# Performance work log

Measured on AMD Instinct MI355X. Metric: run time of the kernel, lower is better.

Reference implementation:

```python
import jax, jax.numpy as jnp
import numpy as np

N_ELEM = 10   # len(EnvPara.ELEMENTS)
N_ATOMS = 100000
N_DIM = 256


def setup_inputs() -> dict:
    key = jax.random.key(0)
    k = jax.random.split(key, 5)
    return {
        "input_tensor": jax.random.normal(k[0], (N_ATOMS, N_DIM), jnp.float32),
        "species": jax.random.randint(k[1], (N_ATOMS,), 0, N_ELEM, dtype=jnp.int64),
        "W1": jax.random.normal(k[2], (N_ELEM, N_DIM, N_DIM), jnp.float32) / np.sqrt(N_DIM).astype(np.float32),
        "b1": jnp.zeros((N_ELEM, N_DIM), jnp.float32),
        "W2": jax.random.normal(k[3], (N_ELEM, N_DIM, 1), jnp.float32) / np.sqrt(N_DIM).astype(np.float32),
        "b2": jnp.zeros((N_ELEM, 1), jnp.float32),
    }


def _element_linear(x, species, W, b):
    # Species-routed linear: each atom uses the weight/bias of its element.
    # Loop over the small fixed element set (N_ELEM=10) to avoid materializing
    # a [n_atoms, d_in, d_out] gathered-weight tensor.
    out = jnp.zeros((x.shape[0], W.shape[2]), dtype=x.dtype)
    for e in range(W.shape[0]):
        mask = (species == e)[:, None]                      # [n_atoms, 1]
        out = out + jnp.where(mask, x @ W[e] + b[e], jnp.zeros((), x.dtype))
    return out


def reference(input_tensor, species, W1, b1, W2, b2):
    # layer2(silu(layer1(x)))
    h = _element_linear(input_tensor, species, W1, b1)      # [n_atoms, n_dim]
    h = jax.nn.silu(h)                                      # way=0 -> plain SiLU
    return _element_linear(h, species, W2, b2)              # [n_atoms, 1]
```

## Files before the change

kernel.cpp:

```cpp
#include <hip/hip_runtime.h>
#include <hip/hip_bf16.h>
#include <stdint.h>


#define NDIM 256
#define CHUNKS 16
#define BCHUNK 16384
#define TROWS 32
#define MAXT 16
#define NB_GEMM 512

typedef __attribute__((ext_vector_type(8))) short short8;
typedef __attribute__((ext_vector_type(8))) unsigned short ushort8;
typedef __attribute__((ext_vector_type(4))) float f32x4;
typedef __attribute__((ext_vector_type(2))) unsigned u32x2;

__device__ __forceinline__ unsigned short f2bf(float f) {
  unsigned u = __float_as_uint(f);
  u = (u + 0x7FFFu + ((u >> 16) & 1u)) >> 16;
  return (unsigned short)u;
}

__device__ __forceinline__ unsigned pk2(float a, float b) {
  return (unsigned)f2bf(a) | ((unsigned)f2bf(b) << 16);
}


__global__ void convw_k(const float* __restrict__ W1, unsigned short* __restrict__ wt, int NE) {
  int t = blockIdx.x * 256 + threadIdx.x;
  if (t >= NE * 8192) return;
  int n = t & 255;
  int g = (t >> 8) & 3;
  int step = (t >> 10) & 7;
  int e = t >> 13;
  int k0 = step * 32 + g * 8;
  const float* src = W1 + ((size_t)e << 16) + (size_t)k0 * NDIM + n;
  unsigned short v[8];
  #pragma unroll
  for (int j = 0; j < 8; ++j) v[j] = f2bf(src[j * NDIM]);
  char* chunk = (char*)wt + (size_t)(e * 8 + step) * BCHUNK;
  unsigned off = ((unsigned)(n * 64 + g * 16)) ^ ((unsigned)((n & 7) << 4));
  *(ushort8*)(chunk + off) = *(ushort8*)v;
}

__global__ void bhist_k(const int* __restrict__ sp, int n, int* __restrict__ bc, int NE) {
  __shared__ int wc[4][16];
  int tid = threadIdx.x;
  int i = blockIdx.x * 256 + tid;
  int s = (i < n) ? sp[i] : -1;
  int w = tid >> 6, lane = tid & 63;
  for (int e = 0; e < NE; ++e) {
    unsigned long long m = __ballot(s == e);
    if (lane == 0) wc[w][e] = __popcll(m);
  }
  __syncthreads();
  if (tid < NE) bc[blockIdx.x * NE + tid] = wc[0][tid] + wc[1][tid] + wc[2][tid] + wc[3][tid];
}

__global__ void scan_k(const int* __restrict__ bc, int* __restrict__ bo,
                       int* __restrict__ atom_start, int* __restrict__ tile_off,
                       int* __restrict__ bstart, int nblocks, int NE) {
  __shared__ int csum[256];
  __shared__ int coff[256];
  __shared__ int stot[16];
  __shared__ int sbase[16];
  int tid = threadIdx.x;
  int per = (nblocks + CHUNKS - 1) / CHUNKS;
  int e = tid / CHUNKS, c = tid % CHUNKS;
  int b0 = c * per, b1 = b0 + per; if (b1 > nblocks) b1 = nblocks;
  if (tid < NE * CHUNKS) {
    int s = 0;
    for (int b = b0; b < b1; ++b) s += bc[b * NE + e];
    csum[tid] = s;
  }
  __syncthreads();
  if (tid < NE) {
    int r = 0;
    for (int c2 = 0; c2 < CHUNKS; ++c2) { coff[tid * CHUNKS + c2] = r; r += csum[tid * CHUNKS + c2]; }
    stot[tid] = r;
  }
  __syncthreads();
  if (tid == 0) {
    int a = 0, t = 0;
    for (int e2 = 0; e2 < NE; ++e2) {
      sbase[e2] = a;
      atom_start[e2] = a; tile_off[e2] = t;
      a += stot[e2]; t += (stot[e2] + TROWS - 1) / TROWS;
    }
    atom_start[NE] = a; tile_off[NE] = t;
    int ntl = t > 0 ? t : 1;
    int nbk[16]; int tot = 0, emax = 0;
    for (int e2 = 0; e2 < NE; ++e2) {
      int nt = tile_off[e2 + 1] - tile_off[e2];
      int v = (nt > 0) ? (int)(((long long)nt * NB_GEMM) / ntl) : 0;
      if (nt > 0 && v < 1) v = 1;
      nbk[e2] = v; tot += v;
      if (nbk[e2] > nbk[emax]) emax = e2;
    }
    nbk[emax] += NB_GEMM - tot;
    int bacc = 0;
    for (int e2 = 0; e2 < NE; ++e2) { bstart[e2] = bacc; bacc += nbk[e2]; }
    bstart[NE] = bacc;
  }
  __syncthreads();
  if (tid < NE * CHUNKS) {
    int run = sbase[e] + coff[tid];
    for (int b = b0; b < b1; ++b) { bo[b * NE + e] = run; run += bc[b * NE + e]; }
  }
}

__global__ void dscatter_k(const int* __restrict__ sp, int n, const int* __restrict__ bo,
                           int* __restrict__ sorted, int NE) {
  __shared__ int wc[4][16];
  int tid = threadIdx.x;
  int i = blockIdx.x * 256 + tid;
  int s = (i < n) ? sp[i] : -1;
  int w = tid >> 6, lane = tid & 63;
  for (int e = 0; e < NE; ++e) {
    unsigned long long m = __ballot(s == e);
    if (lane == 0) wc[w][e] = __popcll(m);
  }
  __syncthreads();
  for (int e = 0; e < NE; ++e) {
    unsigned long long m = __ballot(s == e);
    if (s == e) {
      int wpre = 0;
      for (int w2 = 0; w2 < 4; ++w2) if (w2 < w) wpre += wc[w2][e];
      int rank = __popcll(m & ((1ull << lane) - 1ull));
      sorted[bo[blockIdx.x * NE + e] + wpre + rank] = i;
    }
  }
}


__global__ __launch_bounds__(512, 1) void gemm_k(
    const float* __restrict__ x, const unsigned short* __restrict__ wt,
    const float* __restrict__ b1, const float* __restrict__ w2,
    const float* __restrict__ b2, const int* __restrict__ sorted,
    const int* __restrict__ atom_start, const int* __restrict__ tile_off,
    const int* __restrict__ bstart, float* __restrict__ out, int NE)
{
  __shared__ __align__(16) char ldsT[TROWS * 512];
  __shared__ float partLds[256];
  __shared__ int ldsAtoms[MAXT * TROWS];
  __shared__ int toffs[17], astart[17], bst[17];

  int tid = threadIdx.x, lane = tid & 63, wid = tid >> 6;
  int lr = lane & 15, lg = lane >> 4;

  if (tid <= NE) {
    toffs[tid] = tile_off[tid]; astart[tid] = atom_start[tid]; bst[tid] = bstart[tid];
  }
  __syncthreads();

  int b = blockIdx.x;
  int e = 0;
  while (b >= bst[e + 1]) ++e;
  int j = b - bst[e], nbe = bst[e + 1] - bst[e];
  int nte = toffs[e + 1] - toffs[e];
  int q = nte / nbe, r = nte % nbe;
  int cnt = q + (j < r ? 1 : 0);
  if (cnt <= 0) return;
  if (cnt > MAXT) cnt = MAXT;
  int t0 = toffs[e] + j * q + (j < r ? j : r);
  int t1 = t0 + cnt;

  {
    int rs0 = astart[e] + (t0 - toffs[e]) * TROWS;
    int rvAll = astart[e + 1] - rs0;
    for (int i = tid; i < cnt * TROWS; i += 512) {
      int rloc = (i < rvAll) ? i : (rvAll - 1);
      ldsAtoms[i] = sorted[rs0 + rloc];
    }
  }
  __syncthreads();

  short8 bf[2][8];
  float bbv[2], wvv[2];
  {
    const char* wbase = (const char*)wt + (size_t)e * 8 * BCHUNK;
    #pragma unroll
    for (int nf = 0; nf < 2; ++nf) {
      int ncol = wid * 32 + nf * 16 + lr;
      unsigned off = ((unsigned)(ncol * 64 + lg * 16)) ^ ((unsigned)((ncol & 7) << 4));
      #pragma unroll
      for (int s = 0; s < 8; ++s)
        bf[nf][s] = *(const short8*)(wbase + (size_t)s * BCHUNK + off);
      bbv[nf] = b1[(size_t)e * NDIM + ncol];
      wvv[nf] = w2[(size_t)e * NDIM + ncol];
    }
  }
  float b2v = b2[e];
  #pragma unroll
  for (int nf = 0; nf < 2; ++nf) {
    #pragma unroll
    for (int s = 0; s < 8; ++s) asm volatile("" : "+v"(bf[nf][s]));
    asm volatile("" : "+v"(bbv[nf]), "+v"(wvv[nf]));
  }

  int srow = tid >> 4;
  int skc  = tid & 15;
  unsigned swzW = (unsigned)((srow & 7) << 4);
  unsigned rbW  = (unsigned)(srow * 512 + skc * 8);
  unsigned swzA = (unsigned)((lr & 7) << 4);

  float4 xr0, xr1, xr2, xr3;
  {
    int atom = ldsAtoms[srow];
    const float* xp = x + (size_t)atom * NDIM + skc * 4;
    xr0 = *(const float4*)(xp);
    xr1 = *(const float4*)(xp + 64);
    xr2 = *(const float4*)(xp + 128);
    xr3 = *(const float4*)(xp + 192);
  }

  for (int t = t0; t < t1; ++t) {
    {
      u32x2 w;
      w[0] = pk2(xr0.x, xr0.y); w[1] = pk2(xr0.z, xr0.w);
      *(u32x2*)(ldsT + ((rbW +   0) ^ swzW)) = w;
      w[0] = pk2(xr1.x, xr1.y); w[1] = pk2(xr1.z, xr1.w);
      *(u32x2*)(ldsT + ((rbW + 128) ^ swzW)) = w;
      w[0] = pk2(xr2.x, xr2.y); w[1] = pk2(xr2.z, xr2.w);
      *(u32x2*)(ldsT + ((rbW + 256) ^ swzW)) = w;
      w[0] = pk2(xr3.x, xr3.y); w[1] = pk2(xr3.z, xr3.w);
      *(u32x2*)(ldsT + ((rbW + 384) ^ swzW)) = w;
    }
    if (t + 1 < t1) {
      int atom = ldsAtoms[(t + 1 - t0) * TROWS + srow];
      const float* xp = x + (size_t)atom * NDIM + skc * 4;
      xr0 = *(const float4*)(xp);
      xr1 = *(const float4*)(xp + 64);
      xr2 = *(const float4*)(xp + 128);
      xr3 = *(const float4*)(xp + 192);
    }

    asm volatile("s_waitcnt lgkmcnt(0)" ::: "memory");
    __builtin_amdgcn_s_barrier();
    __builtin_amdgcn_sched_barrier(0);

    f32x4 acc[2][2];
    const f32x4 zero = {0.f, 0.f, 0.f, 0.f};
    #pragma unroll
    for (int i = 0; i < 2; ++i)
      #pragma unroll
      for (int jj = 0; jj < 2; ++jj) acc[i][jj] = zero;

    #pragma unroll
    for (int step = 0; step < 8; ++step) {
      short8 af[2];
      #pragma unroll
      for (int mf = 0; mf < 2; ++mf) {
        unsigned off = ((unsigned)((mf * 16 + lr) * 512 + step * 64 + lg * 16)) ^ swzA;
        af[mf] = *(const short8*)(ldsT + off);
      }
      #pragma unroll
      for (int mf = 0; mf < 2; ++mf)
        #pragma unroll
        for (int nf = 0; nf < 2; ++nf)
          acc[mf][nf] = __builtin_amdgcn_mfma_f32_16x16x32_bf16(af[mf], bf[nf][step], acc[mf][nf], 0, 0, 0);
    }

    float psum[2][4];
    #pragma unroll
    for (int mf = 0; mf < 2; ++mf)
      #pragma unroll
      for (int rg = 0; rg < 4; ++rg) psum[mf][rg] = 0.f;

    #pragma unroll
    for (int nf = 0; nf < 2; ++nf) {
      #pragma unroll
      for (int mf = 0; mf < 2; ++mf)
        #pragma unroll
        for (int rg = 0; rg < 4; ++rg) {
          float h = acc[mf][nf][rg] + bbv[nf];
          float sv = h * __builtin_amdgcn_rcpf(1.f + __expf(-h));
          psum[mf][rg] += sv * wvv[nf];
        }
    }
    #pragma unroll
    for (int mf = 0; mf < 2; ++mf)
      #pragma unroll
      for (int rg = 0; rg < 4; ++rg) {
        float v = psum[mf][rg];
        v += __shfl_xor(v, 1, 64);
        v += __shfl_xor(v, 2, 64);
        v += __shfl_xor(v, 4, 64);
        v += __shfl_xor(v, 8, 64);
        psum[mf][rg] = v;
      }
    if (lr == 0) {
      #pragma unroll
      for (int mf = 0; mf < 2; ++mf)
        #pragma unroll
        for (int rg = 0; rg < 4; ++rg)
          partLds[wid * TROWS + mf * 16 + lg * 4 + rg] = psum[mf][rg];
    }

    asm volatile("s_waitcnt lgkmcnt(0)" ::: "memory");
    __builtin_amdgcn_s_barrier();
    __builtin_amdgcn_sched_barrier(0);

    if (lane < 4) {
      int rloc = wid * 4 + lane;
      float s = b2v;
      #pragma unroll
      for (int w = 0; w < 8; ++w) s += partLds[w * TROWS + rloc];
      out[ldsAtoms[(t - t0) * TROWS + rloc]] = s;
    }
  }
}


extern "C" void kernel_launch(void* const* d_in, const int* in_sizes, int n_in,
                              void* d_out, int out_size, void* d_ws, size_t ws_size,
                              hipStream_t stream) {
  const float* x  = (const float*)d_in[0];
  const int*   sp = (const int*)d_in[1];
  const float* W1 = (const float*)d_in[2];
  const float* b1 = (const float*)d_in[3];
  const float* W2 = (const float*)d_in[4];
  const float* b2 = (const float*)d_in[5];
  float* out = (float*)d_out;

  int n_atoms = in_sizes[0] / NDIM;
  int NE = in_sizes[2] / (NDIM * NDIM);
  int nblocks = (n_atoms + 255) / 256;

  char* wsb = (char*)d_ws;
  size_t o = 0;
  int* bc = (int*)(wsb + o);         o += ((size_t)nblocks * NE * 4 + 255) & ~(size_t)255;
  int* bo = (int*)(wsb + o);         o += ((size_t)nblocks * NE * 4 + 255) & ~(size_t)255;
  int* atom_start = (int*)(wsb + o); o += 256;
  int* tile_off   = (int*)(wsb + o); o += 256;
  int* bstart     = (int*)(wsb + o); o += 256;
  int* sorted     = (int*)(wsb + o); o += ((size_t)n_atoms * 4 + 255) & ~(size_t)255;
  unsigned short* wt = (unsigned short*)(wsb + o);

  hipLaunchKernelGGL(convw_k, dim3((NE * 8192 + 255) / 256), dim3(256), 0, stream,
                     W1, wt, NE);
  hipLaunchKernelGGL(bhist_k, dim3(nblocks), dim3(256), 0, stream, sp, n_atoms, bc, NE);
  hipLaunchKernelGGL(scan_k, dim3(1), dim3(256), 0, stream, bc, bo, atom_start, tile_off,
                     bstart, nblocks, NE);
  hipLaunchKernelGGL(dscatter_k, dim3(nblocks), dim3(256), 0, stream, sp, n_atoms, bo,
                     sorted, NE);

  hipLaunchKernelGGL(gemm_k, dim3(NB_GEMM), dim3(512), 0, stream,
                     x, wt, b1, W2, b2, sorted, atom_start, tile_off, bstart, out, NE);
}
```

Measured before the change: 69.97 us.

## Double GEMM tile rows, swap MFMA operands, and stage weight conversion through LDS

The fused GEMM tile grows from 32 to 64 atom rows and the grid shrinks from 512 to 256 blocks. MFMA operands are swapped so weights form the A side and activations the B side. This lets the SiLU-dot reduction use two cross-lane shuffles instead of four, and lets b1/w2 be held per row group. The weight conversion kernel now loads W1 rows coalesced into LDS and writes transposed bf16 chunks, instead of doing strided per-thread gathers. The larger tile doubles accumulator and x-prefetch registers, and the smaller grid may leave compute units underused.

```diff
diff --git a/kernel.cpp b/kernel.cpp
--- a/kernel.cpp
+++ b/kernel.cpp
@@ -6,9 +6,9 @@
 #define NDIM 256
 #define CHUNKS 16
 #define BCHUNK 16384
-#define TROWS 32
+#define TROWS 64
 #define MAXT 16
-#define NB_GEMM 512
+#define NB_GEMM 256
 
 typedef __attribute__((ext_vector_type(8))) short short8;
 typedef __attribute__((ext_vector_type(8))) unsigned short ushort8;
@@ -27,20 +27,32 @@
 
 
 __global__ void convw_k(const float* __restrict__ W1, unsigned short* __restrict__ wt, int NE) {
-  int t = blockIdx.x * 256 + threadIdx.x;
-  if (t >= NE * 8192) return;
-  int n = t & 255;
-  int g = (t >> 8) & 3;
-  int step = (t >> 10) & 7;
-  int e = t >> 13;
-  int k0 = step * 32 + g * 8;
-  const float* src = W1 + ((size_t)e << 16) + (size_t)k0 * NDIM + n;
-  unsigned short v[8];
-  #pragma unroll
-  for (int j = 0; j < 8; ++j) v[j] = f2bf(src[j * NDIM]);
-  char* chunk = (char*)wt + (size_t)(e * 8 + step) * BCHUNK;
-  unsigned off = ((unsigned)(n * 64 + g * 16)) ^ ((unsigned)((n & 7) << 4));
-  *(ushort8*)(chunk + off) = *(ushort8*)v;
+  __shared__ float ldsW[32 * 260];
+  int blk = blockIdx.x;
+  int e = blk >> 3, step = blk & 7;
+  int tid = threadIdx.x;
+  int k0 = step * 32;
+  {
+    int kk = tid >> 3, part = tid & 7;
+    const float* src = W1 + ((size_t)e << 16) + (size_t)(k0 + kk) * NDIM + part * 32;
+    #pragma unroll
+    for (int j = 0; j < 8; ++j) {
+      float4 v = *(const float4*)(src + j * 4);
+      *(float4*)&ldsW[kk * 260 + part * 32 + j * 4] = v;
+    }
+  }
+  __syncthreads();
+  {
+    int n = tid;
+    unsigned short v[32];
+    #pragma unroll
+    for (int kk = 0; kk < 32; ++kk) v[kk] = f2bf(ldsW[kk * 260 + n]);
+    char* chunk = (char*)wt + (size_t)blk * BCHUNK;
+    unsigned swz = (unsigned)((n & 7) << 4);
+    #pragma unroll
+    for (int g = 0; g < 4; ++g)
+      *(ushort8*)(chunk + (((unsigned)(n * 64 + g * 16)) ^ swz)) = *(ushort8*)&v[g * 8];
+  }
 }
 
 __global__ void bhist_k(const int* __restrict__ sp, int n, int* __restrict__ bc, int NE) {
@@ -141,7 +153,7 @@
     const int* __restrict__ bstart, float* __restrict__ out, int NE)
 {
   __shared__ __align__(16) char ldsT[TROWS * 512];
-  __shared__ float partLds[256];
+  __shared__ float partLds[8 * TROWS];
   __shared__ int ldsAtoms[MAXT * TROWS];
   __shared__ int toffs[17], astart[17], bst[17];
 
@@ -176,137 +188,112 @@
   __syncthreads();
 
   short8 bf[2][8];
-  float bbv[2], wvv[2];
+  float bbv[2][4], wvv[2][4];
   {
     const char* wbase = (const char*)wt + (size_t)e * 8 * BCHUNK;
     #pragma unroll
-    for (int nf = 0; nf < 2; ++nf) {
-      int ncol = wid * 32 + nf * 16 + lr;
+    for (int mf = 0; mf < 2; ++mf) {
+      int ncol = wid * 32 + mf * 16 + lr;
       unsigned off = ((unsigned)(ncol * 64 + lg * 16)) ^ ((unsigned)((ncol & 7) << 4));
       #pragma unroll
       for (int s = 0; s < 8; ++s)
-        bf[nf][s] = *(const short8*)(wbase + (size_t)s * BCHUNK + off);
-      bbv[nf] = b1[(size_t)e * NDIM + ncol];
-      wvv[nf] = w2[(size_t)e * NDIM + ncol];
+        bf[mf][s] = *(const short8*)(wbase + (size_t)s * BCHUNK + off);
+      #pragma unroll
+      for (int rg = 0; rg < 4; ++rg) {
+        int n = wid * 32 + mf * 16 + lg * 4 + rg;
+        bbv[mf][rg] = b1[(size_t)e * NDIM + n];
+        wvv[mf][rg] = w2[(size_t)e * NDIM + n];
+      }
     }
   }
   float b2v = b2[e];
   #pragma unroll
-  for (int nf = 0; nf < 2; ++nf) {
-    #pragma unroll
-    for (int s = 0; s < 8; ++s) asm volatile("" : "+v"(bf[nf][s]));
-    asm volatile("" : "+v"(bbv[nf]), "+v"(wvv[nf]));
-  }
-
-  int srow = tid >> 4;
-  int skc  = tid & 15;
+  for (int mf = 0; mf < 2; ++mf)
+    #pragma unroll
+    for (int s = 0; s < 8; ++s) asm volatile("" : "+v"(bf[mf][s]));
+
+  int srow = tid >> 3;
+  int skc  = tid & 7;
   unsigned swzW = (unsigned)((srow & 7) << 4);
-  unsigned rbW  = (unsigned)(srow * 512 + skc * 8);
-  unsigned swzA = (unsigned)((lr & 7) << 4);
-
-  float4 xr0, xr1, xr2, xr3;
+  float4 xr[8];
   {
     int atom = ldsAtoms[srow];
     const float* xp = x + (size_t)atom * NDIM + skc * 4;
-    xr0 = *(const float4*)(xp);
-    xr1 = *(const float4*)(xp + 64);
-    xr2 = *(const float4*)(xp + 128);
-    xr3 = *(const float4*)(xp + 192);
+    #pragma unroll
+    for (int jj = 0; jj < 8; ++jj) xr[jj] = *(const float4*)(xp + jj * 32);
   }
 
   for (int t = t0; t < t1; ++t) {
-    {
+    #pragma unroll
+    for (int jj = 0; jj < 8; ++jj) {
       u32x2 w;
-      w[0] = pk2(xr0.x, xr0.y); w[1] = pk2(xr0.z, xr0.w);
-      *(u32x2*)(ldsT + ((rbW +   0) ^ swzW)) = w;
-      w[0] = pk2(xr1.x, xr1.y); w[1] = pk2(xr1.z, xr1.w);
-      *(u32x2*)(ldsT + ((rbW + 128) ^ swzW)) = w;
-      w[0] = pk2(xr2.x, xr2.y); w[1] = pk2(xr2.z, xr2.w);
-      *(u32x2*)(ldsT + ((rbW + 256) ^ swzW)) = w;
-      w[0] = pk2(xr3.x, xr3.y); w[1] = pk2(xr3.z, xr3.w);
-      *(u32x2*)(ldsT + ((rbW + 384) ^ swzW)) = w;
+      w[0] = pk2(xr[jj].x, xr[jj].y); w[1] = pk2(xr[jj].z, xr[jj].w);
+      *(u32x2*)(ldsT + (((unsigned)(srow * 512 + jj * 64 + skc * 8)) ^ swzW)) = w;
     }
     if (t + 1 < t1) {
       int atom = ldsAtoms[(t + 1 - t0) * TROWS + srow];
       const float* xp = x + (size_t)atom * NDIM + skc * 4;
-      xr0 = *(const float4*)(xp);
-      xr1 = *(const float4*)(xp + 64);
-      xr2 = *(const float4*)(xp + 128);
-      xr3 = *(const float4*)(xp + 192);
+      #pragma unroll
+      for (int jj = 0; jj < 8; ++jj) xr[jj] = *(const float4*)(xp + jj * 32);
     }
 
     asm volatile("s_waitcnt lgkmcnt(0)" ::: "memory");
     __builtin_amdgcn_s_barrier();
     __builtin_amdgcn_sched_barrier(0);
 
-    f32x4 acc[2][2];
+    f32x4 acc[2][4];
     const f32x4 zero = {0.f, 0.f, 0.f, 0.f};
     #pragma unroll
     for (int i = 0; i < 2; ++i)
       #pragma unroll
-      for (int jj = 0; jj < 2; ++jj) acc[i][jj] = zero;
+      for (int jj = 0; jj < 4; ++jj) acc[i][jj] = zero;
 
     #pragma unroll
     for (int step = 0; step < 8; ++step) {
-      short8 af[2];
-      #pragma unroll
-      for (int mf = 0; mf < 2; ++mf) {
-        unsigned off = ((unsigned)((mf * 16 + lr) * 512 + step * 64 + lg * 16)) ^ swzA;
-        af[mf] = *(const short8*)(ldsT + off);
+      short8 af[4];
+      #pragma unroll
+      for (int nf = 0; nf < 4; ++nf) {
+        unsigned off = ((unsigned)((nf * 16 + lr) * 512 + step * 64 + lg * 16))
+                     ^ ((unsigned)((lr & 7) << 4));
+        af[nf] = *(const short8*)(ldsT + off);
       }
       #pragma unroll
       for (int mf = 0; mf < 2; ++mf)
         #pragma unroll
-        for (int nf = 0; nf < 2; ++nf)
-          acc[mf][nf] = __builtin_amdgcn_mfma_f32_16x16x32_bf16(af[mf], bf[nf][step], acc[mf][nf], 0, 0, 0);
-    }
-
-    float psum[2][4];
-    #pragma unroll
-    for (int mf = 0; mf < 2; ++mf)
-      #pragma unroll
-      for (int rg = 0; rg < 4; ++rg) psum[mf][rg] = 0.f;
-
-    #pragma unroll
-    for (int nf = 0; nf < 2; ++nf) {
+        for (int nf = 0; nf < 4; ++nf)
+          acc[mf][nf] = __builtin_amdgcn_mfma_f32_16x16x32_bf16(bf[mf][step], af[nf], acc[mf][nf], 0, 0, 0);
+    }
+
+    float p[4];
+    #pragma unroll
+    for (int nf = 0; nf < 4; ++nf) {
+      float s = 0.f;
       #pragma unroll
       for (int mf = 0; mf < 2; ++mf)
         #pragma unroll
         for (int rg = 0; rg < 4; ++rg) {
-          float h = acc[mf][nf][rg] + bbv[nf];
-          float sv = h * __builtin_amdgcn_rcpf(1.f + __expf(-h));
-          psum[mf][rg] += sv * wvv[nf];
+          float h = acc[mf][nf][rg] + bbv[mf][rg];
+          s += h * __builtin_amdgcn_rcpf(1.f + __expf(-h)) * wvv[mf][rg];
         }
-    }
-    #pragma unroll
-    for (int mf = 0; mf < 2; ++mf)
-      #pragma unroll
-      for (int rg = 0; rg < 4; ++rg) {
-        float v = psum[mf][rg];
-        v += __shfl_xor(v, 1, 64);
-        v += __shfl_xor(v, 2, 64);
-        v += __shfl_xor(v, 4, 64);
-        v += __shfl_xor(v, 8, 64);
-        psum[mf][rg] = v;
-      }
-    if (lr == 0) {
-      #pragma unroll
-      for (int mf = 0; mf < 2; ++mf)
-        #pragma unroll
-        for (int rg = 0; rg < 4; ++rg)
-          partLds[wid * TROWS + mf * 16 + lg * 4 + rg] = psum[mf][rg];
+      s += __shfl_xor(s, 16, 64);
+      s += __shfl_xor(s, 32, 64);
+      p[nf] = s;
+    }
+    if (lg == 0) {
+      #pragma unroll
+      for (int nf = 0; nf < 4; ++nf)
+        partLds[wid * TROWS + nf * 16 + lr] = p[nf];
     }
 
     asm volatile("s_waitcnt lgkmcnt(0)" ::: "memory");
     __builtin_amdgcn_s_barrier();
     __builtin_amdgcn_sched_barrier(0);
 
-    if (lane < 4) {
-      int rloc = wid * 4 + lane;
+    if (tid < TROWS) {
       float s = b2v;
       #pragma unroll
-      for (int w = 0; w < 8; ++w) s += partLds[w * TROWS + rloc];
-      out[ldsAtoms[(t - t0) * TROWS + rloc]] = s;
+      for (int w = 0; w < 8; ++w) s += partLds[w * TROWS + tid];
+      out[ldsAtoms[(t - t0) * TROWS + tid]] = s;
     }
   }
 }
@@ -337,8 +324,7 @@
   int* sorted     = (int*)(wsb + o); o += ((size_t)n_atoms * 4 + 255) & ~(size_t)255;
   unsigned short* wt = (unsigned short*)(wsb + o);
 
-  hipLaunchKernelGGL(convw_k, dim3((NE * 8192 + 255) / 256), dim3(256), 0, stream,
-                     W1, wt, NE);
+  hipLaunchKernelGGL(convw_k, dim3(NE * 8), dim3(256), 0, stream, W1, wt, NE);
   hipLaunchKernelGGL(bhist_k, dim3(nblocks), dim3(256), 0, stream, sp, n_atoms, bc, NE);
   hipLaunchKernelGGL(scan_k, dim3(1), dim3(256), 0, stream, bc, bo, atom_start, tile_off,
                      bstart, nblocks, NE);
```

Measured after the change: 61.12 us. -12.7%, faster.
